# Optimization experiments

Measured on AMD Instinct MI355X. Metric: run time of the kernel, lower is better.

Reference implementation:

```python
import jax, jax.numpy as jnp
import numpy as np

EMBED_DIM = 1024
HEADS = 16
HEAD_DIM = EMBED_DIM // HEADS
N, SEQ = 2, 2048


def setup_inputs() -> dict:
    key = jax.random.key(0)
    ks = jax.random.split(key, 9)
    s = 1.0 / np.sqrt(HEAD_DIM)
    inp = {
        "values": jax.random.normal(ks[0], (N, SEQ, EMBED_DIM), jnp.float32),
        "keys": jax.random.normal(ks[1], (N, SEQ, EMBED_DIM), jnp.float32),
        "query": jax.random.normal(ks[2], (N, SEQ, EMBED_DIM), jnp.float32),
        "mask": jax.random.randint(ks[3], (N, 1, SEQ, SEQ), 0, 2, jnp.int32),
        # per-head projection weights (torch Linear: y = x @ W.T)
        "Wv": jax.random.normal(ks[4], (HEAD_DIM, HEAD_DIM), jnp.float32) * s,
        "Wk": jax.random.normal(ks[5], (HEAD_DIM, HEAD_DIM), jnp.float32) * s,
        "Wq": jax.random.normal(ks[6], (HEAD_DIM, HEAD_DIM), jnp.float32) * s,
        "Wo": jax.random.normal(ks[7], (EMBED_DIM, EMBED_DIM), jnp.float32) * (1.0 / np.sqrt(EMBED_DIM)),
        "bo": jax.random.normal(ks[8], (EMBED_DIM,), jnp.float32) * 0.01,
    }
    return inp


def reference(values, keys, query, mask, Wv, Wk, Wq, Wo, bo):
    n, q_len = query.shape[0], query.shape[1]
    v_len, k_len = values.shape[1], keys.shape[1]
    # reshape to [N, len, H, D]
    v = values.reshape(n, v_len, HEADS, HEAD_DIM)
    k = keys.reshape(n, k_len, HEADS, HEAD_DIM)
    q = query.reshape(n, q_len, HEADS, HEAD_DIM)
    # per-head linear projections (shared weight across heads), torch: x @ W.T
    v = jnp.einsum("nlhd,ed->nlhe", v, Wv)
    k = jnp.einsum("nlhd,ed->nlhe", k, Wk)
    q = jnp.einsum("nlhd,ed->nlhe", q, Wq)
    # energy: [N, H, Q, K]
    energy = jnp.einsum("nqhd,nkhd->nhqk", q, k)
    energy = jnp.where(mask == 0, jnp.float32(-1e20), energy)
    # NOTE: original scales by sqrt(embed_dim), not sqrt(head_dim)
    attention = jax.nn.softmax(energy / jnp.sqrt(jnp.float32(EMBED_DIM)), axis=3)
    out = jnp.einsum("nhql,nlhd->nqhd", attention, v).reshape(n, q_len, EMBED_DIM)
    out = out @ Wo.T + bo  # fc_out; dropout is identity in eval mode
    return out
```

## Files before the change

kernel.cpp:

```cpp
#include <hip/hip_runtime.h>
#include <hip/hip_bf16.h>

#define NB 2
#define SEQ 2048
#define HEADS 16
#define HD 64
#define ED 1024

typedef __bf16 bf16x8 __attribute__((ext_vector_type(8)));
typedef float f32x4 __attribute__((ext_vector_type(4)));
typedef unsigned short u16x8 __attribute__((ext_vector_type(8)));
typedef unsigned short u16x4 __attribute__((ext_vector_type(4)));

__device__ __forceinline__ unsigned short f2bf(float f) {
    unsigned u = __builtin_bit_cast(unsigned, f);
    u += 0x7fffu + ((u >> 16) & 1u);
    return (unsigned short)(u >> 16);
}

__device__ __forceinline__ bf16x8 cvt8(const float* __restrict__ p) {
    const float4* p4 = (const float4*)p;
    float4 a = p4[0], b = p4[1];
    u16x8 u;
    u[0] = f2bf(a.x); u[1] = f2bf(a.y); u[2] = f2bf(a.z); u[3] = f2bf(a.w);
    u[4] = f2bf(b.x); u[5] = f2bf(b.y); u[6] = f2bf(b.z); u[7] = f2bf(b.w);
    return __builtin_bit_cast(bf16x8, u);
}

__device__ __forceinline__ bf16x8 ldfrag(const void* p) {
    uint4 v = *(const uint4*)p;
    return __builtin_bit_cast(bf16x8, v);
}

__device__ __forceinline__ f32x4 mfma16(bf16x8 a, bf16x8 b, f32x4 c) {
    return __builtin_amdgcn_mfma_f32_16x16x32_bf16(a, b, c, 0, 0, 0);
}

#define GLOAD_LDS(gp, lp) \
    __builtin_amdgcn_global_load_lds( \
        (const __attribute__((address_space(1))) unsigned int*)(gp), \
        (__attribute__((address_space(3))) unsigned int*)(lp), 16, 0, 0)

#define QSCALE 0.04508422f

__global__ __launch_bounds__(256) void mask_bits_kernel(
    const int* __restrict__ mask, unsigned long long* __restrict__ bits)
{
    size_t i = (size_t)blockIdx.x * 256 + threadIdx.x;
    int m = mask[i];
    unsigned long long b = __ballot(m != 0);
    if ((threadIdx.x & 63) == 0) bits[i >> 6] = b;
}

__global__ __launch_bounds__(256) void wo_cvt_kernel(
    const float* __restrict__ Wo, unsigned short* __restrict__ Wob)
{
    size_t i = ((size_t)blockIdx.x * 256 + threadIdx.x) * 4;
    float4 v = *(const float4*)(Wo + i);
    u16x4 u;
    u[0] = f2bf(v.x); u[1] = f2bf(v.y); u[2] = f2bf(v.z); u[3] = f2bf(v.w);
    *(u16x4*)(Wob + i) = u;
}

__global__ __launch_bounds__(256) void proj_kernel(
    const float* __restrict__ qin, const float* __restrict__ kin, const float* __restrict__ vin,
    const float* __restrict__ Wq, const float* __restrict__ Wk, const float* __restrict__ Wv,
    unsigned short* __restrict__ Qb, unsigned short* __restrict__ Kb,
    unsigned short* __restrict__ Vt)
{
    __shared__ __align__(16) char tile[64 * 144];

    int t3  = blockIdx.x >> 10;
    int rem = blockIdx.x & 1023;
    int h   = rem >> 6;
    int rt  = rem & 63;
    int wave = threadIdx.x >> 6, lane = threadIdx.x & 63;
    int quad = lane >> 4, l16 = lane & 15;

    const float* in = (t3 == 0) ? qin : ((t3 == 1) ? kin : vin);
    const float* W  = (t3 == 0) ? Wq  : ((t3 == 1) ? Wk  : Wv);

    int r0 = rt * 64 + wave * 16;

    bf16x8 bf0[4], bf1[4];
#pragma unroll
    for (int sl = 0; sl < 4; ++sl) {
        const float* wrow = W + (sl * 16 + l16) * 64;
        bf0[sl] = cvt8(wrow + quad * 8);
        bf1[sl] = cvt8(wrow + 32 + quad * 8);
    }
    const float* xrow = in + (size_t)(r0 + l16) * ED + h * 64;
    bf16x8 af0 = cvt8(xrow + quad * 8);
    bf16x8 af1 = cvt8(xrow + 32 + quad * 8);

    f32x4 acc[4];
#pragma unroll
    for (int sl = 0; sl < 4; ++sl) {
        f32x4 c = {0.f, 0.f, 0.f, 0.f};
        c = mfma16(af0, bf0[sl], c);
        c = mfma16(af1, bf1[sl], c);
        acc[sl] = c;
    }
    float sc = (t3 == 0) ? QSCALE : 1.0f;

    size_t nh = (size_t)((r0 >> 11) * HEADS + h);
    int rl = lane >> 3, cl = lane & 7;

    if (t3 != 2) {
#pragma unroll
        for (int r = 0; r < 4; ++r) {
            int srow = wave * 16 + quad * 4 + r;
#pragma unroll
            for (int sl = 0; sl < 4; ++sl)
                *(unsigned short*)(tile + srow * 144 + (sl * 16 + l16) * 2) =
                    f2bf(acc[sl][r] * sc);
        }
        unsigned short* dst = (t3 == 0) ? Qb : Kb;
        int s0 = (r0 & 2047);
#pragma unroll
        for (int g = 0; g < 2; ++g) {
            int lrow = wave * 16 + g * 8 + rl;
            uint4 v = *(const uint4*)(tile + lrow * 144 + cl * 16);
            *(uint4*)(dst + (nh * SEQ + (s0 & ~15) + g * 8 + rl) * HD + cl * 8) = v;
        }
    } else {
#pragma unroll
        for (int r = 0; r < 4; ++r) {
            int srow = wave * 16 + quad * 4 + r;
#pragma unroll
            for (int sl = 0; sl < 4; ++sl)
                *(unsigned short*)(tile + (sl * 16 + l16) * 144 + srow * 2) =
                    f2bf(acc[sl][r]);
        }
        __syncthreads();
        int s_tile = rt & 31;
#pragma unroll
        for (int g = 0; g < 2; ++g) {
            int erow = wave * 16 + g * 8 + rl;
            uint4 v = *(const uint4*)(tile + erow * 144 + cl * 16);
            *(uint4*)(Vt + ((nh * 32 + s_tile) * 64 + erow) * 64 + cl * 8) = v;
        }
    }
}

template <int SPLIT>
__global__ __launch_bounds__(256) void attn_kernel(
    const unsigned short* __restrict__ Qb, const unsigned short* __restrict__ Kb,
    const unsigned short* __restrict__ Vt2, const unsigned long long* __restrict__ mb,
    unsigned short* __restrict__ Ab, float* __restrict__ Of, float* __restrict__ Ls)
{
    __shared__ __align__(16) char smem[8192 + 8192 + 4 * 4608];

    int tid = threadIdx.x;
    int wave = tid >> 6, lane = tid & 63;
    int quad = lane >> 4, l16 = lane & 15;

    int b   = blockIdx.x;
    int xcd = b & 7;
    int j   = b >> 3;
    int nh, qb, half;
    if (SPLIT) { nh = xcd * 4 + (j >> 5); int r = j & 31; qb = r >> 1; half = r & 1; }
    else       { nh = xcd * 4 + (j >> 4); qb = j & 15; half = 0; }
    int n = nh >> 4, h = nh & 15;
    int q0 = qb * 128 + wave * 32;

    size_t headoff = (size_t)nh * SEQ * HD;
    bf16x8 qf[2][2];
#pragma unroll
    for (int t = 0; t < 2; ++t) {
        const unsigned short* qrow = Qb + headoff + (size_t)(q0 + t * 16 + l16) * HD;
        qf[t][0] = ldfrag(qrow + quad * 8);
        qf[t][1] = ldfrag(qrow + 32 + quad * 8);
    }

    int srow = lane >> 3, sslot = lane & 7;
    int stoff = srow * 128 + (((sslot - srow) & 7) * 16);

    int rotA = ((quad + l16) & 7) * 16;
    int aK  = l16 * 128 + rotA;
    int aKx = aK ^ 64;
    int aV  = 8192 + l16 * 128 + rotA;
    int aVx = aV ^ 64;
    char* pbase = smem + 16384 + wave * 4608;

    const unsigned short* gK = Kb + headoff;
    const unsigned short* gV = Vt2 + (size_t)nh * (32 * 4096);
    const unsigned long long* mbase = mb + (size_t)n * (SEQ * SEQ / 64)
                                         + (size_t)(q0 + quad * 4) * (SEQ / 64);

    f32x4 o[2][4] = {{{0,0,0,0},{0,0,0,0},{0,0,0,0},{0,0,0,0}},
                     {{0,0,0,0},{0,0,0,0},{0,0,0,0},{0,0,0,0}}};
    float lsum[2][4] = {{0,0,0,0},{0,0,0,0}};

    int kb0   = SPLIT ? half * (SEQ / 2) : 0;
    int kbend = SPLIT ? kb0 + (SEQ / 2) : SEQ;

    for (int kb = kb0; kb < kbend; kb += 64) {
        __syncthreads();
        const char* srcK = (const char*)(gK + (size_t)kb * 64) + stoff;
        const char* srcV = (const char*)(gV + (size_t)(kb >> 6) * 4096) + stoff;
#pragma unroll
        for (int i = 0; i < 4; ++i) {
            int c = wave * 4 + i;
            if (c < 8) GLOAD_LDS(srcK + c * 1024, smem + c * 1024);
            else       GLOAD_LDS(srcV + (c - 8) * 1024, smem + 8192 + (c - 8) * 1024);
        }
        unsigned long long m64[2][4];
#pragma unroll
        for (int t = 0; t < 2; ++t)
#pragma unroll
            for (int r = 0; r < 4; ++r)
                m64[t][r] = mbase[(size_t)(t * 16 + r) * (SEQ / 64) + (kb >> 6)] >> l16;
        __syncthreads();

        bf16x8 kf[4][2];
#pragma unroll
        for (int kt = 0; kt < 4; ++kt) {
            kf[kt][0] = ldfrag(smem + aK  + kt * 2048);
            kf[kt][1] = ldfrag(smem + aKx + kt * 2048);
        }
#pragma unroll
        for (int t = 0; t < 2; ++t) {
            f32x4 c[4];
#pragma unroll
            for (int kt = 0; kt < 4; ++kt) {
                f32x4 cc = {0.f, 0.f, 0.f, 0.f};
                cc = mfma16(qf[t][0], kf[kt][0], cc);
                cc = mfma16(qf[t][1], kf[kt][1], cc);
                c[kt] = cc;
            }
            char* pw = pbase + t * 2304 + quad * 576 + l16 * 2;
#pragma unroll
            for (int r = 0; r < 4; ++r) {
                unsigned mlo = (unsigned)m64[t][r];
                unsigned mhi = (unsigned)(m64[t][r] >> 32);
                float p0 = (mlo & 1u)       ? __builtin_exp2f(c[0][r]) : 0.f;
                float p1 = (mlo & 0x10000u) ? __builtin_exp2f(c[1][r]) : 0.f;
                float p2 = (mhi & 1u)       ? __builtin_exp2f(c[2][r]) : 0.f;
                float p3 = (mhi & 0x10000u) ? __builtin_exp2f(c[3][r]) : 0.f;
                lsum[t][r] += (p0 + p1) + (p2 + p3);
                *(unsigned short*)(pw + r * 144)      = (unsigned short)((__builtin_bit_cast(unsigned, p0) + 0x8000u) >> 16);
                *(unsigned short*)(pw + r * 144 + 32) = (unsigned short)((__builtin_bit_cast(unsigned, p1) + 0x8000u) >> 16);
                *(unsigned short*)(pw + r * 144 + 64) = (unsigned short)((__builtin_bit_cast(unsigned, p2) + 0x8000u) >> 16);
                *(unsigned short*)(pw + r * 144 + 96) = (unsigned short)((__builtin_bit_cast(unsigned, p3) + 0x8000u) >> 16);
            }
        }
#pragma unroll
        for (int t = 0; t < 2; ++t) {
            char* pr = pbase + t * 2304 + l16 * 144 + quad * 16;
            bf16x8 pf0 = ldfrag(pr);
            bf16x8 pf1 = ldfrag(pr + 64);
#pragma unroll
            for (int sl = 0; sl < 4; ++sl) {
                o[t][sl] = mfma16(pf0, ldfrag(smem + aV  + sl * 2048), o[t][sl]);
                o[t][sl] = mfma16(pf1, ldfrag(smem + aVx + sl * 2048), o[t][sl]);
            }
        }
    }

#pragma unroll
    for (int t = 0; t < 2; ++t) {
#pragma unroll
        for (int r = 0; r < 4; ++r) {
            float s = lsum[t][r];
            s += __shfl_xor(s, 1);
            s += __shfl_xor(s, 2);
            s += __shfl_xor(s, 4);
            s += __shfl_xor(s, 8);
            int qrowi = q0 + t * 16 + quad * 4 + r;
            if (SPLIT) {
                size_t qg = (size_t)nh * SEQ + qrowi;
                if (l16 == 0) Ls[(size_t)half * 65536 + qg] = s;
                float* op = Of + ((size_t)half * 65536 + qg) * 64;
#pragma unroll
                for (int sl = 0; sl < 4; ++sl)
                    op[sl * 16 + l16] = o[t][sl][r];
            } else {
                float rinv = 1.0f / s;
                size_t obase = ((size_t)(n * SEQ + qrowi) * HEADS + h) * HD;
#pragma unroll
                for (int sl = 0; sl < 4; ++sl)
                    Ab[obase + sl * 16 + l16] = f2bf(o[t][sl][r] * rinv);
            }
        }
    }
}

__global__ __launch_bounds__(256) void combine_kernel(
    const float* __restrict__ Of, const float* __restrict__ Ls,
    unsigned short* __restrict__ Ab)
{
    int idx = blockIdx.x * 256 + threadIdx.x;
    int q  = idx >> 4;
    int d0 = (idx & 15) * 4;
    const float4 o0 = *(const float4*)(Of + (size_t)q * 64 + d0);
    const float4 o1 = *(const float4*)(Of + 4194304 + (size_t)q * 64 + d0);
    float rl = 1.0f / (Ls[q] + Ls[65536 + q]);
    int n = q >> 15, h = (q >> 11) & 15, s = q & 2047;
    size_t ab = (((size_t)(n * SEQ + s)) * HEADS + h) * HD + d0;
    u16x4 u;
    u[0] = f2bf((o0.x + o1.x) * rl);
    u[1] = f2bf((o0.y + o1.y) * rl);
    u[2] = f2bf((o0.z + o1.z) * rl);
    u[3] = f2bf((o0.w + o1.w) * rl);
    *(u16x4*)(Ab + ab) = u;
}

__global__ __launch_bounds__(256) void out_gemm_kernel(
    const unsigned short* __restrict__ Ab, const unsigned short* __restrict__ Wob,
    const float* __restrict__ bo, float* __restrict__ out)
{
    __shared__ __align__(16) char lds[32768];

    int wave = threadIdx.x >> 6, lane = threadIdx.x & 63;
    int quad = lane >> 4, l16 = lane & 15;
    int rt = blockIdx.x >> 3, ct = blockIdx.x & 7;
    int wr = wave >> 1, wc = wave & 1;

    int srow = lane >> 3, sslot = lane & 7;
    int stoff = srow * 2048 + (((sslot - srow) & 7) * 16);
    const char* gA = (const char*)Ab  + (size_t)rt * 128 * 2048 + stoff;
    const char* gB = (const char*)Wob + (size_t)ct * 128 * 2048 + stoff;

    int aA[4], aB[4];
#pragma unroll
    for (int i = 0; i < 4; ++i) {
        int rowA = wr * 64 + i * 16 + l16;
        aA[i] = rowA * 128 + (((quad + rowA) & 7) * 16);
        int rowB = wc * 64 + i * 16 + l16;
        aB[i] = 16384 + rowB * 128 + (((quad + rowB) & 7) * 16);
    }

    f32x4 acc[4][4] = {};
    for (int f = 0; f < ED; f += 64) {
        __syncthreads();
#pragma unroll
        for (int i = 0; i < 4; ++i) {
            int c = wave * 4 + i;
            GLOAD_LDS(gA + (size_t)c * 16384 + f * 2, lds + c * 1024);
            GLOAD_LDS(gB + (size_t)c * 16384 + f * 2, lds + 16384 + c * 1024);
        }
        __syncthreads();
#pragma unroll
        for (int kk = 0; kk < 2; ++kk) {
            int x = kk * 64;
            bf16x8 af[4], bfr[4];
#pragma unroll
            for (int i = 0; i < 4; ++i)  af[i]  = ldfrag(lds + (aA[i] ^ x));
#pragma unroll
            for (int sl = 0; sl < 4; ++sl) bfr[sl] = ldfrag(lds + (aB[sl] ^ x));
#pragma unroll
            for (int i = 0; i < 4; ++i)
#pragma unroll
                for (int sl = 0; sl < 4; ++sl)
                    acc[i][sl] = mfma16(af[i], bfr[sl], acc[i][sl]);
        }
    }

    float bv[4];
#pragma unroll
    for (int sl = 0; sl < 4; ++sl)
        bv[sl] = bo[ct * 128 + wc * 64 + sl * 16 + l16];
#pragma unroll
    for (int i = 0; i < 4; ++i)
#pragma unroll
        for (int r = 0; r < 4; ++r) {
            int row = rt * 128 + wr * 64 + i * 16 + quad * 4 + r;
#pragma unroll
            for (int sl = 0; sl < 4; ++sl) {
                int e = ct * 128 + wc * 64 + sl * 16 + l16;
                out[(size_t)row * ED + e] = acc[i][sl][r] + bv[sl];
            }
        }
}

extern "C" void kernel_launch(void* const* d_in, const int* in_sizes, int n_in,
                              void* d_out, int out_size, void* d_ws, size_t ws_size,
                              hipStream_t stream)
{
    const float* values = (const float*)d_in[0];
    const float* keys   = (const float*)d_in[1];
    const float* query  = (const float*)d_in[2];
    const int*   mask   = (const int*)d_in[3];
    const float* Wv     = (const float*)d_in[4];
    const float* Wk     = (const float*)d_in[5];
    const float* Wq     = (const float*)d_in[6];
    const float* Wo     = (const float*)d_in[7];
    const float* bo     = (const float*)d_in[8];
    float* out = (float*)d_out;

    char* w = (char*)d_ws;
    unsigned short* Qb  = (unsigned short*)(w);
    unsigned short* Kb  = (unsigned short*)(w +  8388608);
    unsigned short* Vt  = (unsigned short*)(w + 16777216);
    unsigned short* Ab  = (unsigned short*)(w + 25165824);
    unsigned long long* Mb = (unsigned long long*)(w + 33554432);
    unsigned short* Wob = (unsigned short*)(w + 34603008);
    float* Of = (float*)(w + 36700160);
    float* Ls = (float*)(w + 70254592);

    bool split = ws_size >= 70778880ULL;

    mask_bits_kernel<<<NB * SEQ * SEQ / 256, 256, 0, stream>>>(mask, Mb);
    wo_cvt_kernel<<<ED * ED / (256 * 4), 256, 0, stream>>>(Wo, Wob);
    proj_kernel<<<3 * HEADS * 64, 256, 0, stream>>>(query, keys, values, Wq, Wk, Wv, Qb, Kb, Vt);
    if (split) {
        attn_kernel<1><<<1024, 256, 0, stream>>>(Qb, Kb, Vt, Mb, Ab, Of, Ls);
        combine_kernel<<<4096, 256, 0, stream>>>(Of, Ls, Ab);
    } else {
        attn_kernel<0><<<512, 256, 0, stream>>>(Qb, Kb, Vt, Mb, Ab, Of, Ls);
    }
    out_gemm_kernel<<<256, 256, 0, stream>>>(Ab, Wob, bo, out);
}
```

Baseline: 260.1 us.

## Transpose attention MFMA operands so each lane owns one query row

Swaps the MFMA operand order in both the QK^T and PV products so results come out transposed: each lane holds one query row across four key columns. Each lane then needs one mask word per tile instead of four, the row sum reduces across quads with two shuffles instead of four per row, P is written to LDS as packed 8-byte stores rather than 2-byte stores, and outputs are written as vectors. The PV loop is reordered so V fragments are loaded once per slice and reused for both query tiles. This relies on the transposed fragment layouts and mask bit offsets being consistent.

```diff
diff --git a/kernel.cpp b/kernel.cpp
--- a/kernel.cpp
+++ b/kernel.cpp
@@ -34,6 +34,12 @@
 
 __device__ __forceinline__ f32x4 mfma16(bf16x8 a, bf16x8 b, f32x4 c) {
     return __builtin_amdgcn_mfma_f32_16x16x32_bf16(a, b, c, 0, 0, 0);
+}
+
+__device__ __forceinline__ unsigned packbf(float lo, float hi) {
+    unsigned a = __builtin_bit_cast(unsigned, lo) + 0x8000u;
+    unsigned b = __builtin_bit_cast(unsigned, hi) + 0x8000u;
+    return (b & 0xFFFF0000u) | (a >> 16);
 }
 
 #define GLOAD_LDS(gp, lp) \
@@ -182,15 +188,18 @@
     int aV  = 8192 + l16 * 128 + rotA;
     int aVx = aV ^ 64;
     char* pbase = smem + 16384 + wave * 4608;
+    char* pw = pbase + l16 * 144 + quad * 8;
+    char* pr = pbase + l16 * 144 + quad * 16;
 
     const unsigned short* gK = Kb + headoff;
     const unsigned short* gV = Vt2 + (size_t)nh * (32 * 4096);
     const unsigned long long* mbase = mb + (size_t)n * (SEQ * SEQ / 64)
-                                         + (size_t)(q0 + quad * 4) * (SEQ / 64);
+                                         + (size_t)(q0 + l16) * (SEQ / 64);
 
     f32x4 o[2][4] = {{{0,0,0,0},{0,0,0,0},{0,0,0,0},{0,0,0,0}},
                      {{0,0,0,0},{0,0,0,0},{0,0,0,0},{0,0,0,0}}};
-    float lsum[2][4] = {{0,0,0,0},{0,0,0,0}};
+    float lsum[2] = {0.f, 0.f};
+    int qsh = quad * 4;
 
     int kb0   = SPLIT ? half * (SEQ / 2) : 0;
     int kbend = SPLIT ? kb0 + (SEQ / 2) : SEQ;
@@ -205,12 +214,10 @@
             if (c < 8) GLOAD_LDS(srcK + c * 1024, smem + c * 1024);
             else       GLOAD_LDS(srcV + (c - 8) * 1024, smem + 8192 + (c - 8) * 1024);
         }
-        unsigned long long m64[2][4];
+        unsigned long long m64[2];
 #pragma unroll
         for (int t = 0; t < 2; ++t)
-#pragma unroll
-            for (int r = 0; r < 4; ++r)
-                m64[t][r] = mbase[(size_t)(t * 16 + r) * (SEQ / 64) + (kb >> 6)] >> l16;
+            m64[t] = mbase[(size_t)(t * 16) * (SEQ / 64) + (kb >> 6)] >> qsh;
         __syncthreads();
 
         bf16x8 kf[4][2];
@@ -225,62 +232,71 @@
 #pragma unroll
             for (int kt = 0; kt < 4; ++kt) {
                 f32x4 cc = {0.f, 0.f, 0.f, 0.f};
-                cc = mfma16(qf[t][0], kf[kt][0], cc);
-                cc = mfma16(qf[t][1], kf[kt][1], cc);
+                cc = mfma16(kf[kt][0], qf[t][0], cc);
+                cc = mfma16(kf[kt][1], qf[t][1], cc);
                 c[kt] = cc;
             }
-            char* pw = pbase + t * 2304 + quad * 576 + l16 * 2;
-#pragma unroll
-            for (int r = 0; r < 4; ++r) {
-                unsigned mlo = (unsigned)m64[t][r];
-                unsigned mhi = (unsigned)(m64[t][r] >> 32);
-                float p0 = (mlo & 1u)       ? __builtin_exp2f(c[0][r]) : 0.f;
-                float p1 = (mlo & 0x10000u) ? __builtin_exp2f(c[1][r]) : 0.f;
-                float p2 = (mhi & 1u)       ? __builtin_exp2f(c[2][r]) : 0.f;
-                float p3 = (mhi & 0x10000u) ? __builtin_exp2f(c[3][r]) : 0.f;
-                lsum[t][r] += (p0 + p1) + (p2 + p3);
-                *(unsigned short*)(pw + r * 144)      = (unsigned short)((__builtin_bit_cast(unsigned, p0) + 0x8000u) >> 16);
-                *(unsigned short*)(pw + r * 144 + 32) = (unsigned short)((__builtin_bit_cast(unsigned, p1) + 0x8000u) >> 16);
-                *(unsigned short*)(pw + r * 144 + 64) = (unsigned short)((__builtin_bit_cast(unsigned, p2) + 0x8000u) >> 16);
-                *(unsigned short*)(pw + r * 144 + 96) = (unsigned short)((__builtin_bit_cast(unsigned, p3) + 0x8000u) >> 16);
-            }
-        }
+            unsigned mlo = (unsigned)m64[t];
+            unsigned mhi = (unsigned)(m64[t] >> 32);
+            float ls = 0.f;
+#pragma unroll
+            for (int kt = 0; kt < 4; ++kt) {
+                unsigned mw = (kt & 2) ? mhi : mlo;
+                int bs = (kt & 1) ? 16 : 0;
+                float p0 = ((mw >> (bs + 0)) & 1u) ? __builtin_exp2f(c[kt][0]) : 0.f;
+                float p1 = ((mw >> (bs + 1)) & 1u) ? __builtin_exp2f(c[kt][1]) : 0.f;
+                float p2 = ((mw >> (bs + 2)) & 1u) ? __builtin_exp2f(c[kt][2]) : 0.f;
+                float p3 = ((mw >> (bs + 3)) & 1u) ? __builtin_exp2f(c[kt][3]) : 0.f;
+                ls += (p0 + p1) + (p2 + p3);
+                uint2 dw = { packbf(p0, p1), packbf(p2, p3) };
+                *(uint2*)(pw + t * 2304 + kt * 32) = dw;
+            }
+            lsum[t] += ls;
+        }
+        bf16x8 pb[2][2];
 #pragma unroll
         for (int t = 0; t < 2; ++t) {
-            char* pr = pbase + t * 2304 + l16 * 144 + quad * 16;
-            bf16x8 pf0 = ldfrag(pr);
-            bf16x8 pf1 = ldfrag(pr + 64);
+            pb[t][0] = ldfrag(pr + t * 2304);
+            pb[t][1] = ldfrag(pr + t * 2304 + 64);
+        }
+#pragma unroll
+        for (int sl = 0; sl < 4; ++sl) {
+            bf16x8 va0 = ldfrag(smem + aV  + sl * 2048);
+            bf16x8 va1 = ldfrag(smem + aVx + sl * 2048);
+#pragma unroll
+            for (int t = 0; t < 2; ++t) {
+                o[t][sl] = mfma16(va0, pb[t][0], o[t][sl]);
+                o[t][sl] = mfma16(va1, pb[t][1], o[t][sl]);
+            }
+        }
+    }
+
+#pragma unroll
+    for (int t = 0; t < 2; ++t) {
+        float s = lsum[t];
+        s += __shfl_xor(s, 16);
+        s += __shfl_xor(s, 32);
+        int q = q0 + t * 16 + l16;
+        if (SPLIT) {
+            size_t qg = (size_t)nh * SEQ + q;
+            if (quad == 0) Ls[(size_t)half * 65536 + qg] = s;
+            float* op = Of + ((size_t)half * 65536 + qg) * 64 + qsh;
 #pragma unroll
             for (int sl = 0; sl < 4; ++sl) {
-                o[t][sl] = mfma16(pf0, ldfrag(smem + aV  + sl * 2048), o[t][sl]);
-                o[t][sl] = mfma16(pf1, ldfrag(smem + aVx + sl * 2048), o[t][sl]);
-            }
-        }
-    }
-
-#pragma unroll
-    for (int t = 0; t < 2; ++t) {
-#pragma unroll
-        for (int r = 0; r < 4; ++r) {
-            float s = lsum[t][r];
-            s += __shfl_xor(s, 1);
-            s += __shfl_xor(s, 2);
-            s += __shfl_xor(s, 4);
-            s += __shfl_xor(s, 8);
-            int qrowi = q0 + t * 16 + quad * 4 + r;
-            if (SPLIT) {
-                size_t qg = (size_t)nh * SEQ + qrowi;
-                if (l16 == 0) Ls[(size_t)half * 65536 + qg] = s;
-                float* op = Of + ((size_t)half * 65536 + qg) * 64;
-#pragma unroll
-                for (int sl = 0; sl < 4; ++sl)
-                    op[sl * 16 + l16] = o[t][sl][r];
-            } else {
-                float rinv = 1.0f / s;
-                size_t obase = ((size_t)(n * SEQ + qrowi) * HEADS + h) * HD;
-#pragma unroll
-                for (int sl = 0; sl < 4; ++sl)
-                    Ab[obase + sl * 16 + l16] = f2bf(o[t][sl][r] * rinv);
+                float4 v = { o[t][sl][0], o[t][sl][1], o[t][sl][2], o[t][sl][3] };
+                *(float4*)(op + sl * 16) = v;
+            }
+        } else {
+            float rinv = 1.0f / s;
+            unsigned short* op = Ab + (((size_t)(n * SEQ + q)) * HEADS + h) * HD + qsh;
+#pragma unroll
+            for (int sl = 0; sl < 4; ++sl) {
+                u16x4 u;
+                u[0] = f2bf(o[t][sl][0] * rinv);
+                u[1] = f2bf(o[t][sl][1] * rinv);
+                u[2] = f2bf(o[t][sl][2] * rinv);
+                u[3] = f2bf(o[t][sl][3] * rinv);
+                *(u16x4*)(op + sl * 16) = u;
             }
         }
     }
```

New measurement: 258.2 us. About the same (-0.7%).
